# Optimization experiments

Measured on AMD Instinct MI355X. Metric: run time of the kernel, lower is better.

## Reference

```python
import jax, jax.numpy as jnp
import numpy as np

# Static config matching init_kwargs / input_specs
B, C, H, W, T = 2, 128, 32, 32, 32
OUT = 256
WS, SHIFT, HEADS = 4, 2, 8
MLP = 4 * C
N = WS ** 3          # tokens per 4x4x4 window = 64
D_BLOCKS = 4         # depth=2 -> 2 (no-shift, shift) pairs


def _rel_idx():
    coords = np.stack(np.meshgrid(np.arange(WS), np.arange(WS), np.arange(WS), indexing='ij')).reshape(3, -1)
    rel = (coords[:, :, None] - coords[:, None, :]).transpose(1, 2, 0) + (WS - 1)
    return (rel[..., 0] * (2 * WS - 1) ** 2 + rel[..., 1] * (2 * WS - 1) + rel[..., 2]).astype(np.int32)

REL_IDX = jnp.asarray(_rel_idx())  # [N, N]


def _attn_mask():
    # Faithful port of Block.createmask (H,W,T already multiples of WS)
    img = np.zeros((H, W, T))
    sl = (slice(0, -WS), slice(-WS, -SHIFT), slice(-SHIFT, None))
    cnt = 0
    for hs in sl:
        for ws_ in sl:
            for ts in sl:
                img[hs, ws_, ts] = cnt
                cnt += 1
    m = img.reshape(H // WS, WS, W // WS, WS, T // WS, WS).transpose(0, 2, 4, 1, 3, 5).reshape(-1, N)
    am = m[:, None, :] - m[:, :, None]
    return jnp.asarray(np.where(am != 0, -100.0, 0.0).astype(np.float32))  # [nW, N, N]

MASK = _attn_mask()


def _partition(x):  # [b,H,W,T,c] -> [b*nW, N, c]
    b, c = x.shape[0], x.shape[-1]
    x = x.reshape(b, H // WS, WS, W // WS, WS, T // WS, WS, c).transpose(0, 1, 3, 5, 2, 4, 6, 7)
    return x.reshape(-1, N, c)


def _reverse(wins, b, c):  # [b*nW, N, c] -> [b,H,W,T,c]
    x = wins.reshape(b, H // WS, W // WS, T // WS, WS, WS, WS, c).transpose(0, 1, 4, 2, 5, 3, 6, 7)
    return x.reshape(b, H, W, T, c)


def _ln(x, g, b):
    mu = x.mean(-1, keepdims=True)
    var = ((x - mu) ** 2).mean(-1, keepdims=True)
    return (x - mu) / jnp.sqrt(var + 1e-5) * g + b


def _swin(x, shift, g1, b1, qw, qb, pw, pb, rpb, g2, b2, f1w, f1b, f2w, f2b):
    b, L, c = x.shape
    hd = c // HEADS
    scale = hd ** -0.5
    h = _ln(x, g1, b1).reshape(b, H, W, T, c)
    if shift:
        h = jnp.roll(h, (-SHIFT, -SHIFT, -SHIFT), axis=(1, 2, 3))
    win = _partition(h)  # [b*nW, N, c]
    qkv = (win @ qw.T + qb).reshape(-1, N, 3, HEADS, hd).transpose(2, 0, 3, 1, 4)
    q, k, v = qkv[0] * scale, qkv[1], qkv[2]
    attn = jnp.einsum('bhnd,bhmd->bhnm', q, k) + rpb[REL_IDX].transpose(2, 0, 1)[None]
    if shift:
        nW = MASK.shape[0]
        attn = (attn.reshape(b, nW, HEADS, N, N) + MASK[None, :, None]).reshape(-1, HEADS, N, N)
    attn = jax.nn.softmax(attn, axis=-1)
    o = jnp.einsum('bhnm,bhmd->bhnd', attn, v).transpose(0, 2, 1, 3).reshape(-1, N, c)
    o = o @ pw.T + pb
    h = _reverse(o, b, c)
    if shift:
        h = jnp.roll(h, (SHIFT, SHIFT, SHIFT), axis=(1, 2, 3))
    x = x + h.reshape(b, L, c)
    m = jax.nn.gelu(_ln(x, g2, b2) @ f1w.T + f1b, approximate=False)
    return x + (m @ f2w.T + f2b)


def setup_inputs() -> dict:
    key = jax.random.key(0)
    ks = jax.random.split(key, 10)
    r = lambda i, sh, s=0.02: jax.random.normal(ks[i], sh, jnp.float32) * s
    Dn = D_BLOCKS
    return {
        'x': jax.random.normal(ks[0], (B, C, H, W, T), jnp.float32),
        'norm1_g': jnp.ones((Dn, C), jnp.float32), 'norm1_b': jnp.zeros((Dn, C), jnp.float32),
        'qkv_w': r(1, (Dn, 3 * C, C)), 'qkv_b': jnp.zeros((Dn, 3 * C), jnp.float32),
        'proj_w': r(2, (Dn, C, C)), 'proj_b': jnp.zeros((Dn, C), jnp.float32),
        'rpb': r(3, (Dn, (2 * WS - 1) ** 3, HEADS)),
        'norm2_g': jnp.ones((Dn, C), jnp.float32), 'norm2_b': jnp.zeros((Dn, C), jnp.float32),
        'fc1_w': r(4, (Dn, MLP, C)), 'fc1_b': jnp.zeros((Dn, MLP), jnp.float32),
        'fc2_w': r(5, (Dn, C, MLP)), 'fc2_b': jnp.zeros((Dn, C), jnp.float32),
        'dw_w': r(6, (C, 1, 3, 3, 3), 0.1), 'dw_b': jnp.zeros((C,), jnp.float32),
        'pw_w': r(7, (OUT, C, 1, 1, 1), 0.05), 'pw_b': jnp.zeros((OUT,), jnp.float32),
        'bn_g': jnp.ones((OUT,), jnp.float32), 'bn_b': jnp.zeros((OUT,), jnp.float32),
    }


def reference(x, norm1_g, norm1_b, qkv_w, qkv_b, proj_w, proj_b, rpb, norm2_g, norm2_b,
              fc1_w, fc1_b, fc2_w, fc2_b, dw_w, dw_b, pw_w, pw_b, bn_g, bn_b):
    b = x.shape[0]
    t = x.transpose(0, 2, 3, 4, 1).reshape(b, H * W * T, C)  # b (h w t) c
    shifts = [0, SHIFT, 0, SHIFT]
    for i, s in enumerate(shifts):
        t = _swin(t, s, norm1_g[i], norm1_b[i], qkv_w[i], qkv_b[i], proj_w[i], proj_b[i],
                  rpb[i], norm2_g[i], norm2_b[i], fc1_w[i], fc1_b[i], fc2_w[i], fc2_b[i])
    y = t.reshape(b, H, W, T, C).transpose(0, 4, 1, 2, 3)
    # connectBlock: depthwise 3x3x3 conv + pointwise 1x1x1 conv + BatchNorm3d + ReLU
    dn = ('NCDHW', 'OIDHW', 'NCDHW')
    y = jax.lax.conv_general_dilated(y, dw_w, (1, 1, 1), 'SAME', dimension_numbers=dn,
                                     feature_group_count=C) + dw_b[None, :, None, None, None]
    y = jax.lax.conv_general_dilated(y, pw_w, (1, 1, 1), 'SAME', dimension_numbers=dn) + pw_b[None, :, None, None, None]
    mu = y.mean((0, 2, 3, 4), keepdims=True)
    var = ((y - mu) ** 2).mean((0, 2, 3, 4), keepdims=True)
    y = (y - mu) / jnp.sqrt(var + 1e-5) * bn_g[None, :, None, None, None] + bn_b[None, :, None, None, None]
    return jax.nn.relu(y)
```

## Files before the change

kernel.cpp:

```cpp
#include <hip/hip_runtime.h>
#include <hip/hip_bf16.h>
#include <cstddef>
#include <cstdint>

typedef __attribute__((ext_vector_type(8))) short short8;
typedef __attribute__((ext_vector_type(4))) short short4v;
typedef __attribute__((ext_vector_type(4))) float floatx4;
typedef __hip_bfloat16 bf16;

#define HEADS 8
#define TOK   65536
#define OUTC  256

__device__ inline float b2f(short s) {
    union { unsigned u; float f; } x;
    x.u = ((unsigned)(unsigned short)s) << 16;
    return x.f;
}

__device__ inline floatx4 mfma16(short4v a, short4v b, floatx4 c) {
#if __has_builtin(__builtin_amdgcn_mfma_f32_16x16x16bf16_1k)
    return __builtin_amdgcn_mfma_f32_16x16x16bf16_1k(a, b, c, 0, 0, 0);
#else
    floatx4 d;
    asm volatile("v_mfma_f32_16x16x16_bf16 %0, %1, %2, %3\n\ts_nop 7"
                 : "=v"(d) : "v"(a), "v"(b), "v"(c));
    return d;
#endif
}

__global__ __launch_bounds__(256) void transpose_in_kernel(
    const float* __restrict__ x, float* __restrict__ out, float* __restrict__ tstats)
{
    __shared__ float tile[128 * 65];
    int chunk = blockIdx.x;
    int tid = threadIdx.x;
    int b = chunk >> 9;
    int sp0 = (chunk & 511) * 64;
    #pragma unroll
    for (int l = 0; l < 32; ++l) {
        int idx = l * 256 + tid;
        int c = idx >> 6;
        int s = idx & 63;
        tile[c * 65 + s] = x[(((size_t)(b * 128 + c)) << 15) + sp0 + s];
    }
    __syncthreads();
    #pragma unroll
    for (int l = 0; l < 32; ++l) {
        int idx = l * 256 + tid;
        int s = idx >> 7;
        int c = idx & 127;
        out[((size_t)((b << 15) + sp0 + s)) * 128 + c] = tile[c * 65 + s];
    }
    int s = tid >> 2, q = tid & 3;
    float sm = 0.f, sq = 0.f;
    #pragma unroll
    for (int cc = 0; cc < 32; ++cc) {
        float v = tile[(q * 32 + cc) * 65 + s];
        sm += v; sq += v * v;
    }
    sm += __shfl_xor(sm, 1); sq += __shfl_xor(sq, 1);
    sm += __shfl_xor(sm, 2); sq += __shfl_xor(sq, 2);
    if (q == 0) {
        float mu = sm * (1.0f / 128.0f);
        float var = sq * (1.0f / 128.0f) - mu * mu;
        size_t tok = (size_t)(b << 15) + sp0 + s;
        tstats[tok * 2]     = mu;
        tstats[tok * 2 + 1] = rsqrtf(var + 1e-5f);
    }
}

__global__ __launch_bounds__(256) void prep_kernel(
    const float* __restrict__ qkv_w, const float* __restrict__ proj_w,
    const float* __restrict__ fc1_w, const float* __restrict__ fc2_w,
    const float* __restrict__ pw_w, const float* __restrict__ dw_w,
    const float* __restrict__ norm1_g,
    bf16* __restrict__ wbf, float* __restrict__ dwt, float* __restrict__ stats)
{
    int i = blockIdx.x * 256 + threadIdx.x;
    float v;
    if (i < 196608) {
        int layer = i / 49152, k = i & 127;
        v = qkv_w[i] * norm1_g[layer * 128 + k];
    }
    else if (i < 262144)  v = proj_w[i - 196608];
    else if (i < 524288)  v = fc1_w[i - 262144];
    else if (i < 786432)  v = fc2_w[i - 524288];
    else                  v = pw_w[i - 786432];
    wbf[i] = __float2bfloat16(v);
    if (i < 3456) {
        int c = i / 27, k = i % 27;
        dwt[k * 128 + c] = dw_w[i];
    }
    if (i < 512) stats[i] = 0.f;
}

__global__ __launch_bounds__(256) void foldbias_kernel(
    const float* __restrict__ qkv_w, const float* __restrict__ qkv_b,
    const float* __restrict__ norm1_b, float* __restrict__ qkvb)
{
    int t = blockIdx.x * 256 + threadIdx.x;
    if (t >= 1536) return;
    int l = t / 384, n = t % 384;
    const float* wr = qkv_w + (size_t)l * 49152 + n * 128;
    const float* br = norm1_b + l * 128;
    float s = qkv_b[t];
    #pragma unroll 4
    for (int k = 0; k < 128; ++k) s += wr[k] * br[k];
    qkvb[t] = s;
}

__global__ __launch_bounds__(256) void pack_kernel(
    const float* __restrict__ fc1_w, const float* __restrict__ fc2_w,
    bf16* __restrict__ pw1, bf16* __restrict__ pw2)
{
    int t = blockIdx.x * 256 + threadIdx.x;
    int i = t >> 17;
    int rem = t & 131071;
    int type = rem >> 16;
    int idx = rem & 65535;
    int j = idx & 7, lane = (idx >> 3) & 63;
    int ln15 = lane & 15, quad = lane >> 4;
    if (type == 0) {
        int nt = (idx >> 9) & 1, kk = (idx >> 10) & 3, wv = (idx >> 12) & 3, cc = (idx >> 14) & 3;
        int row = cc * 128 + wv * 32 + nt * 16 + ln15;
        int col = kk * 32 + quad * 8 + j;
        pw1[i * 65536 + idx] = __float2bfloat16(fc1_w[(size_t)i * 65536 + row * 128 + col]);
    } else {
        int nt = (idx >> 9) & 1, ks = (idx >> 10) & 3, cc = (idx >> 12) & 3, wv = (idx >> 14) & 3;
        int row = wv * 32 + nt * 16 + ln15;
        int col = cc * 128 + ks * 32 + quad * 8 + j;
        pw2[i * 65536 + idx] = __float2bfloat16(fc2_w[(size_t)i * 65536 + row * 512 + col]);
    }
}

__global__ __launch_bounds__(256) void rpe_expand_kernel(
    const float* __restrict__ rpb, float* __restrict__ rpe, int layer)
{
    int t = blockIdx.x * 256 + threadIdx.x;
    int j = t & 63, i = (t >> 6) & 63, head = (t >> 12) & 7, wt = t >> 15;
    int ih = i >> 4, iw = (i >> 2) & 3, it = i & 3;
    int jh = j >> 4, jw = (j >> 2) & 3, jt = j & 3;
    int ridx = ((ih - jh + 3) * 7 + (iw - jw + 3)) * 7 + (it - jt + 3);
    float v = rpb[layer * 2744 + ridx * 8 + head];
    if (wt) {
        bool ok = true;
        if (wt & 4) ok = ok && ((ih >= 2) == (jh >= 2));
        if (wt & 2) ok = ok && ((iw >= 2) == (jw >= 2));
        if (wt & 1) ok = ok && ((it >= 2) == (jt >= 2));
        if (!ok) v -= 100.f;
    }
    rpe[t] = v;
}

__global__ __launch_bounds__(256) void gemm_bf16_kernel(
    const bf16* __restrict__ A, const bf16* __restrict__ Bw,
    const float* __restrict__ bias, bf16* __restrict__ Cb, float* __restrict__ Cf,
    float* __restrict__ aux, const float* __restrict__ p1, const float* __restrict__ p2,
    int M, int N, int K, int mode, int shift)
{
    __shared__ __align__(16) char smem[34816];
    __shared__ float cs[128];
    __shared__ float cq[128];
    short* As = (short*)smem;
    short* Bs = (short*)(smem + 8192);
    int tid = threadIdx.x;
    int lane = tid & 63, wv = tid >> 6;
    int wm = wv >> 1, wn = wv & 1;
    int ln15 = lane & 15, quad = lane >> 4;
    int q8 = quad * 8;
    int nBase = blockIdx.x * 128;
    int mBase = blockIdx.y * 128;
    floatx4 acc[4][4] = {};

    if (mode == 4 && tid < 128) { cs[tid] = 0.f; cq[tid] = 0.f; }

    int srow = tid >> 2, scb = tid & 3;

    int toks[2]; float tmu[2], trs[2];
    if (mode == 0) {
        #pragma unroll
        for (int i = 0; i < 2; ++i) {
            int m = mBase + srow + i * 64;
            int n = m & 63, w = (m >> 6) & 511, b = m >> 15;
            int ih = n >> 4, iw = (n >> 2) & 3, it = n & 3;
            int wh = w >> 6, ww = (w >> 3) & 7, wt = w & 7;
            int h  = (wh * 4 + ih + shift) & 31;
            int w2 = (ww * 4 + iw + shift) & 31;
            int t  = (wt * 4 + it + shift) & 31;
            toks[i] = (b << 15) + ((h * 32 + w2) * 32 + t);
            tmu[i] = aux[(size_t)toks[i] * 2];
            trs[i] = aux[(size_t)toks[i] * 2 + 1];
        }
    }

    for (int k0 = 0; k0 < K; k0 += 32) {
        if (mode == 0) {
            int cb = k0 + scb * 8;
            #pragma unroll
            for (int i = 0; i < 2; ++i) {
                const float* xr = Cf + (size_t)toks[i] * 128 + cb;
                float4 a0 = *(const float4*)xr;
                float4 a1 = *(const float4*)(xr + 4);
                float mu = tmu[i], rs = trs[i];
                __align__(16) bf16 pk[8];
                pk[0] = __float2bfloat16((a0.x - mu) * rs);
                pk[1] = __float2bfloat16((a0.y - mu) * rs);
                pk[2] = __float2bfloat16((a0.z - mu) * rs);
                pk[3] = __float2bfloat16((a0.w - mu) * rs);
                pk[4] = __float2bfloat16((a1.x - mu) * rs);
                pk[5] = __float2bfloat16((a1.y - mu) * rs);
                pk[6] = __float2bfloat16((a1.z - mu) * rs);
                pk[7] = __float2bfloat16((a1.w - mu) * rs);
                ((uint4*)As)[i * 256 + tid] = *(const uint4*)pk;
                ((uint4*)Bs)[i * 256 + tid] =
                    *(const uint4*)(Bw + (size_t)(nBase + srow + i * 64) * K + cb);
            }
        } else {
            #pragma unroll
            for (int i = 0; i < 2; ++i) {
                int row = srow + i * 64;
                ((uint4*)As)[i * 256 + tid] =
                    *(const uint4*)(A + (size_t)(mBase + row) * K + k0 + scb * 8);
                ((uint4*)Bs)[i * 256 + tid] =
                    *(const uint4*)(Bw + (size_t)(nBase + row) * K + k0 + scb * 8);
            }
        }
        __syncthreads();
        short8 af[4], bfr[4];
        #pragma unroll
        for (int mt = 0; mt < 4; ++mt)
            af[mt] = *(const short8*)&As[(wm * 64 + mt * 16 + ln15) * 32 + q8];
        #pragma unroll
        for (int nt = 0; nt < 4; ++nt)
            bfr[nt] = *(const short8*)&Bs[(wn * 64 + nt * 16 + ln15) * 32 + q8];
        #pragma unroll
        for (int mt = 0; mt < 4; ++mt)
            #pragma unroll
            for (int nt = 0; nt < 4; ++nt)
                acc[mt][nt] = __builtin_amdgcn_mfma_f32_16x16x32_bf16(
                    af[mt], bfr[nt], acc[mt][nt], 0, 0, 0);
        __syncthreads();
    }

    if (mode == 4) {
        #pragma unroll
        for (int nt = 0; nt < 4; ++nt) {
            int nl = wn * 64 + nt * 16 + ln15;
            float bs = bias[nBase + nl];
            float s = 0.f, sq = 0.f;
            #pragma unroll
            for (int mt = 0; mt < 4; ++mt)
                #pragma unroll
                for (int r = 0; r < 4; ++r) {
                    float v = acc[mt][nt][r] + bs;
                    s += v; sq += v * v;
                }
            atomicAdd(&cs[nl], s);
            atomicAdd(&cq[nl], sq);
        }
        __syncthreads();
        if (tid < 128) {
            atomicAdd(&aux[nBase + tid], cs[tid]);
            atomicAdd(&aux[256 + nBase + tid], cq[tid]);
        }
        return;
    }

    if (mode == 0) {
        bf16* estage = (bf16*)smem;
        float qsc = (nBase == 0) ? 0.25f : 1.0f;
        #pragma unroll
        for (int mt = 0; mt < 4; ++mt)
            #pragma unroll
            for (int nt = 0; nt < 4; ++nt)
                #pragma unroll
                for (int r = 0; r < 4; ++r) {
                    int row = wm * 64 + mt * 16 + quad * 4 + r;
                    int col = wn * 64 + nt * 16 + ln15;
                    estage[row * 136 + col] =
                        __float2bfloat16((acc[mt][nt][r] + bias[nBase + col]) * qsc);
                }
        __syncthreads();
        int row = tid >> 1, hf = tid & 1;
        #pragma unroll
        for (int j = 0; j < 4; ++j) {
            int col = hf * 64 + j * 16;
            *(uint4*)(Cb + (size_t)(mBase + row) * N + nBase + col) =
                *(const uint4*)&estage[row * 136 + col];
            *(uint4*)(Cb + (size_t)(mBase + row) * N + nBase + col + 8) =
                *(const uint4*)&estage[row * 136 + col + 8];
        }
        return;
    }

    if (mode == 2) {
        float* fstage = (float*)smem;
        #pragma unroll
        for (int hf = 0; hf < 2; ++hf) {
            if (wm == hf) {
                #pragma unroll
                for (int mt = 0; mt < 4; ++mt)
                    #pragma unroll
                    for (int nt = 0; nt < 4; ++nt)
                        #pragma unroll
                        for (int r = 0; r < 4; ++r) {
                            int ml = mt * 16 + quad * 4 + r;
                            int col = wn * 64 + nt * 16 + ln15;
                            fstage[ml * 132 + col] = acc[mt][nt][r] + bias[col];
                        }
            }
            __syncthreads();
            int tl = tid >> 2, part = tid & 3;
            int g = mBase + hf * 64 + tl;
            int n_ = g & 63, w = (g >> 6) & 511, b = g >> 15;
            int ih = n_ >> 4, iw = (n_ >> 2) & 3, it = n_ & 3;
            int wh = w >> 6, ww = (w >> 3) & 7, wt = w & 7;
            int h  = (wh * 4 + ih + shift) & 31;
            int w2 = (ww * 4 + iw + shift) & 31;
            int t  = (wt * 4 + it + shift) & 31;
            size_t tok = ((size_t)b << 15) + ((h * 32 + w2) * 32 + t);
            float* dst = aux + tok * 128 + part * 32;
            #pragma unroll
            for (int j = 0; j < 8; ++j) {
                float4 a = *(float4*)(dst + j * 4);
                float4 l = *(const float4*)&fstage[tl * 132 + part * 32 + j * 4];
                a.x += l.x; a.y += l.y; a.z += l.z; a.w += l.w;
                *(float4*)(dst + j * 4) = a;
            }
            __syncthreads();
        }
        return;
    }

    {
        float* fstage = (float*)smem;
        int b = mBase >> 15, sp0 = mBase & 32767;
        #pragma unroll
        for (int hf = 0; hf < 2; ++hf) {
            if (wn == hf) {
                #pragma unroll
                for (int nt = 0; nt < 4; ++nt) {
                    int ncol = nt * 16 + ln15;
                    int nn = nBase + hf * 64 + ncol;
                    float mean = aux[nn] * (1.0f / 65536.0f);
                    float var  = aux[256 + nn] * (1.0f / 65536.0f) - mean * mean;
                    float sc = rsqrtf(var + 1e-5f) * p1[nn];
                    float off = p2[nn] + bias[nn] * sc - mean * sc;
                    #pragma unroll
                    for (int mt = 0; mt < 4; ++mt)
                        #pragma unroll
                        for (int r = 0; r < 4; ++r) {
                            int ml = wm * 64 + mt * 16 + quad * 4 + r;
                            float y = acc[mt][nt][r] * sc + off;
                            fstage[ncol * 132 + ml] = fmaxf(y, 0.f);
                        }
                }
            }
            __syncthreads();
            int nl = tid >> 2, part = tid & 3;
            int nn = nBase + hf * 64 + nl;
            float* dst = Cf + (((size_t)(b * 256 + nn)) << 15) + sp0 + part * 32;
            #pragma unroll
            for (int j = 0; j < 8; ++j)
                *(float4*)(dst + j * 4) = *(const float4*)&fstage[nl * 132 + part * 32 + j * 4];
            __syncthreads();
        }
    }
}

__global__ __launch_bounds__(256, 4) void mlp_kernel(
    float* __restrict__ xbuf, const float* __restrict__ g, const float* __restrict__ bta,
    const bf16* __restrict__ pw1, const float* __restrict__ b1,
    const bf16* __restrict__ pw2, const float* __restrict__ b2,
    bf16* __restrict__ xout16, float* __restrict__ tstats)
{
    __shared__ __align__(16) bf16 smem[64 * 136 * 2];
    bf16* aln  = smem;
    bf16* hidc = smem + 64 * 136;
    float* ostage = (float*)smem;
    int tid = threadIdx.x;
    int lane = tid & 63, wv = tid >> 6;
    int ln15 = lane & 15, quad = lane >> 4;
    int q8 = quad * 8;
    size_t tok0 = (size_t)blockIdx.x * 64;

    #pragma unroll
    for (int itk = 0; itk < 16; ++itk) {
        int t = wv * 16 + itk;
        const float* xp = xbuf + (tok0 + t) * 128;
        float v0 = xp[lane], v1 = xp[lane + 64];
        float s = v0 + v1, sq = v0 * v0 + v1 * v1;
        #pragma unroll
        for (int o = 32; o > 0; o >>= 1) { s += __shfl_xor(s, o); sq += __shfl_xor(sq, o); }
        float mu  = s * (1.0f / 128.0f);
        float var = sq * (1.0f / 128.0f) - mu * mu;
        float rs  = rsqrtf(var + 1e-5f);
        aln[t * 136 + lane]      = __float2bfloat16((v0 - mu) * rs * g[lane]      + bta[lane]);
        aln[t * 136 + lane + 64] = __float2bfloat16((v1 - mu) * rs * g[lane + 64] + bta[lane + 64]);
    }
    __syncthreads();

    floatx4 acc2[4][2] = {};
    #pragma unroll
    for (int cc = 0; cc < 4; ++cc) {
        floatx4 acc[4][2] = {};
        const bf16* p1w = pw1 + (size_t)(cc * 4 + wv) * 4096;
        #pragma unroll
        for (int kk = 0; kk < 4; ++kk) {
            short8 af[4], bfr[2];
            #pragma unroll
            for (int mt = 0; mt < 4; ++mt)
                af[mt] = *(const short8*)&aln[(mt * 16 + ln15) * 136 + kk * 32 + q8];
            #pragma unroll
            for (int nt = 0; nt < 2; ++nt)
                bfr[nt] = *(const short8*)(p1w + kk * 1024 + nt * 512 + lane * 8);
            #pragma unroll
            for (int mt = 0; mt < 4; ++mt)
                #pragma unroll
                for (int nt = 0; nt < 2; ++nt)
                    acc[mt][nt] = __builtin_amdgcn_mfma_f32_16x16x32_bf16(
                        af[mt], bfr[nt], acc[mt][nt], 0, 0, 0);
        }
        if (cc) __syncthreads();
        #pragma unroll
        for (int mt = 0; mt < 4; ++mt)
            #pragma unroll
            for (int nt = 0; nt < 2; ++nt)
                #pragma unroll
                for (int r = 0; r < 4; ++r) {
                    int m = mt * 16 + quad * 4 + r;
                    int ncl = wv * 32 + nt * 16 + ln15;
                    float v = acc[mt][nt][r] + b1[cc * 128 + ncl];
                    float u = v * (0.7978845608f + 0.0356774081f * v * v);
                    v = v * __builtin_amdgcn_rcpf(1.f + __expf(-2.f * u));
                    hidc[m * 136 + ncl] = __float2bfloat16(v);
                }
        __syncthreads();
        const bf16* p2w = pw2 + (size_t)(wv * 4 + cc) * 4096;
        #pragma unroll
        for (int ks = 0; ks < 4; ++ks) {
            short8 af[4], bfr[2];
            #pragma unroll
            for (int mt = 0; mt < 4; ++mt)
                af[mt] = *(const short8*)&hidc[(mt * 16 + ln15) * 136 + ks * 32 + q8];
            #pragma unroll
            for (int nt = 0; nt < 2; ++nt)
                bfr[nt] = *(const short8*)(p2w + ks * 1024 + nt * 512 + lane * 8);
            #pragma unroll
            for (int mt = 0; mt < 4; ++mt)
                #pragma unroll
                for (int nt = 0; nt < 2; ++nt)
                    acc2[mt][nt] = __builtin_amdgcn_mfma_f32_16x16x32_bf16(
                        af[mt], bfr[nt], acc2[mt][nt], 0, 0, 0);
        }
    }
    __syncthreads();

    #pragma unroll
    for (int mt = 0; mt < 4; ++mt)
        #pragma unroll
        for (int nt = 0; nt < 2; ++nt)
            #pragma unroll
            for (int r = 0; r < 4; ++r) {
                int m = mt * 16 + quad * 4 + r;
                int n = wv * 32 + nt * 16 + ln15;
                ostage[m * 132 + n] = acc2[mt][nt][r] + b2[n];
            }
    __syncthreads();

    #pragma unroll
    for (int jj = 0; jj < 8; ++jj) {
        int idx = (jj * 256 + tid) * 4;
        int t = idx >> 7, c = idx & 127;
        float4 v = *(const float4*)(xbuf + tok0 * 128 + idx);
        float4 o = *(const float4*)&ostage[t * 132 + c];
        v.x += o.x; v.y += o.y; v.z += o.z; v.w += o.w;
        *(float4*)(xbuf + tok0 * 128 + idx) = v;
        if (xout16) {
            __align__(8) bf16 hh[4];
            hh[0] = __float2bfloat16(v.x); hh[1] = __float2bfloat16(v.y);
            hh[2] = __float2bfloat16(v.z); hh[3] = __float2bfloat16(v.w);
            *(uint2*)(xout16 + tok0 * 128 + idx) = *(const uint2*)hh;
        }
        float ps = v.x + v.y + v.z + v.w;
        float pq = v.x * v.x + v.y * v.y + v.z * v.z + v.w * v.w;
        #pragma unroll
        for (int o2 = 16; o2 > 0; o2 >>= 1) {
            ps += __shfl_xor(ps, o2); pq += __shfl_xor(pq, o2);
        }
        if ((tid & 31) == 0) {
            float mu = ps * (1.0f / 128.0f);
            float var = pq * (1.0f / 128.0f) - mu * mu;
            size_t tok = tok0 + t;
            tstats[tok * 2]     = mu;
            tstats[tok * 2 + 1] = rsqrtf(var + 1e-5f);
        }
    }
}

__global__ __launch_bounds__(256, 3) void attn_mfma_kernel(
    const bf16* __restrict__ qkv, const float* __restrict__ rpe,
    bf16* __restrict__ outp, int shift)
{
    __shared__ __align__(16) short qs[64 * 392];
    int tid = threadIdx.x;
    int lane = tid & 63, wv = tid >> 6;
    int ln15 = lane & 15, quad = lane >> 4;
    int win = blockIdx.x;
    size_t tok0 = (size_t)win * 64;

    const short* gq = (const short*)qkv + tok0 * 384;
    #pragma unroll
    for (int l = 0; l < 12; ++l) {
        int idx = l * 256 + tid;
        int r = idx / 48, c = idx - r * 48;
        *(uint4*)&qs[r * 392 + c * 8] = *(const uint4*)&gq[r * 384 + c * 8];
    }
    int w = win & 511;
    int wtype = 0;
    if (shift)
        wtype = (((w >> 6) == 7) << 2) | ((((w >> 3) & 7) == 7) << 1) | (int)((w & 7) == 7);
    const float* rpw = rpe + ((size_t)(wtype * 8) << 12);
    __syncthreads();

    floatx4 oacc[2][4];
    #pragma unroll
    for (int hh = 0; hh < 2; ++hh) {
        int head = wv * 2 + hh;
        const float* rph = rpw + ((size_t)head << 12);

        floatx4 acc[4][4];
        #pragma unroll
        for (int jt = 0; jt < 4; ++jt)
            #pragma unroll
            for (int it = 0; it < 4; ++it)
                acc[jt][it] = *(const floatx4*)&rph[(it * 16 + ln15) * 64 + jt * 16 + quad * 4];

        short4v qf[4], kf[4];
        #pragma unroll
        for (int it = 0; it < 4; ++it)
            qf[it] = *(const short4v*)&qs[(it * 16 + ln15) * 392 + head * 16 + quad * 4];
        #pragma unroll
        for (int jt = 0; jt < 4; ++jt)
            kf[jt] = *(const short4v*)&qs[(jt * 16 + ln15) * 392 + 128 + head * 16 + quad * 4];

        #pragma unroll
        for (int jt = 0; jt < 4; ++jt)
            #pragma unroll
            for (int it = 0; it < 4; ++it)
                acc[jt][it] = mfma16(kf[jt], qf[it], acc[jt][it]);

        short4v pf[4][4];
        #pragma unroll
        for (int it = 0; it < 4; ++it) {
            float m = -1e30f;
            #pragma unroll
            for (int jt = 0; jt < 4; ++jt)
                #pragma unroll
                for (int r = 0; r < 4; ++r) m = fmaxf(m, acc[jt][it][r]);
            m = fmaxf(m, __shfl_xor(m, 16));
            m = fmaxf(m, __shfl_xor(m, 32));
            float s = 0.f;
            #pragma unroll
            for (int jt = 0; jt < 4; ++jt)
                #pragma unroll
                for (int r = 0; r < 4; ++r) {
                    float e = __expf(acc[jt][it][r] - m);
                    acc[jt][it][r] = e; s += e;
                }
            s += __shfl_xor(s, 16);
            s += __shfl_xor(s, 32);
            float inv = 1.0f / s;
            #pragma unroll
            for (int jt = 0; jt < 4; ++jt) {
                __align__(8) bf16 pb[4];
                #pragma unroll
                for (int r = 0; r < 4; ++r)
                    pb[r] = __float2bfloat16(acc[jt][it][r] * inv);
                pf[jt][it] = *(const short4v*)pb;
            }
        }

        short4v vf[4];
        #pragma unroll
        for (int jt = 0; jt < 4; ++jt)
            #pragma unroll
            for (int jj = 0; jj < 4; ++jj)
                vf[jt][jj] = qs[(jt * 16 + quad * 4 + jj) * 392 + 256 + head * 16 + ln15];

        #pragma unroll
        for (int it = 0; it < 4; ++it) {
            floatx4 o = {0.f, 0.f, 0.f, 0.f};
            #pragma unroll
            for (int jt = 0; jt < 4; ++jt)
                o = mfma16(vf[jt], pf[jt][it], o);
            oacc[hh][it] = o;
        }
    }
    __syncthreads();

    short* ob = qs;
    #pragma unroll
    for (int hh = 0; hh < 2; ++hh)
        #pragma unroll
        for (int it = 0; it < 4; ++it) {
            __align__(8) bf16 t4[4];
            #pragma unroll
            for (int r = 0; r < 4; ++r) t4[r] = __float2bfloat16(oacc[hh][it][r]);
            *(short4v*)&ob[(it * 16 + ln15) * 136 + (wv * 2 + hh) * 16 + quad * 4] =
                *(const short4v*)t4;
        }
    __syncthreads();

    short* po = (short*)outp + tok0 * 128;
    #pragma unroll
    for (int l = 0; l < 4; ++l) {
        int idx = l * 256 + tid;
        int r = idx >> 4, c = idx & 15;
        *(uint4*)&po[r * 128 + c * 8] = *(const uint4*)&ob[r * 136 + c * 8];
    }
}

__global__ __launch_bounds__(256) void dwconv_kernel(
    const bf16* __restrict__ x, const float* __restrict__ dwt,
    const float* __restrict__ bias, bf16* __restrict__ out)
{
    int blk = blockIdx.x;
    int b = blk >> 9;
    int h = (blk >> 4) & 31;
    int w = ((blk & 15) << 1) | (threadIdx.x >> 7);
    int tid = threadIdx.x & 127;
    int c0 = (tid & 31) * 4;
    int t0 = (tid >> 5) * 8;

    float4 acc[8];
    float4 bs = *(const float4*)&bias[c0];
    #pragma unroll
    for (int o = 0; o < 8; ++o) acc[o] = bs;

    #pragma unroll
    for (int kh = 0; kh < 3; ++kh) {
        int hh = h + kh - 1;
        if (hh < 0 || hh > 31) continue;
        #pragma unroll
        for (int kw = 0; kw < 3; ++kw) {
            int ww = w + kw - 1;
            if (ww < 0 || ww > 31) continue;
            const short* px = (const short*)x +
                ((size_t)(b << 15) + (hh * 32 + ww) * 32) * 128 + c0;
            float4 v[10];
            #pragma unroll
            for (int u = 0; u < 10; ++u) {
                int tt = t0 - 1 + u;
                if (tt >= 0 && tt < 32) {
                    short4v s4 = *(const short4v*)(px + (size_t)tt * 128);
                    v[u].x = b2f(s4[0]); v[u].y = b2f(s4[1]);
                    v[u].z = b2f(s4[2]); v[u].w = b2f(s4[3]);
                } else {
                    v[u].x = v[u].y = v[u].z = v[u].w = 0.f;
                }
            }
            int kb = kh * 9 + kw * 3;
            float4 w0 = *(const float4*)&dwt[(kb + 0) * 128 + c0];
            float4 w1 = *(const float4*)&dwt[(kb + 1) * 128 + c0];
            float4 w2 = *(const float4*)&dwt[(kb + 2) * 128 + c0];
            #pragma unroll
            for (int o = 0; o < 8; ++o) {
                acc[o].x += v[o].x * w0.x + v[o + 1].x * w1.x + v[o + 2].x * w2.x;
                acc[o].y += v[o].y * w0.y + v[o + 1].y * w1.y + v[o + 2].y * w2.y;
                acc[o].z += v[o].z * w0.z + v[o + 1].z * w1.z + v[o + 2].z * w2.z;
                acc[o].w += v[o].w * w0.w + v[o + 1].w * w1.w + v[o + 2].w * w2.w;
            }
        }
    }
    short* po = (short*)out + ((size_t)(b << 15) + (h * 32 + w) * 32 + t0) * 128 + c0;
    #pragma unroll
    for (int o = 0; o < 8; ++o) {
        __align__(8) bf16 h4[4];
        h4[0] = __float2bfloat16(acc[o].x);
        h4[1] = __float2bfloat16(acc[o].y);
        h4[2] = __float2bfloat16(acc[o].z);
        h4[3] = __float2bfloat16(acc[o].w);
        *(uint2*)(po + (size_t)o * 128) = *(const uint2*)h4;
    }
}

extern "C" void kernel_launch(void* const* d_in, const int* in_sizes, int n_in,
                              void* d_out, int out_size, void* d_ws, size_t ws_size,
                              hipStream_t stream)
{
    const float* x_in    = (const float*)d_in[0];
    const float* norm1_g = (const float*)d_in[1];
    const float* norm1_b = (const float*)d_in[2];
    const float* qkv_w   = (const float*)d_in[3];
    const float* qkv_b   = (const float*)d_in[4];
    const float* proj_w  = (const float*)d_in[5];
    const float* proj_b  = (const float*)d_in[6];
    const float* rpb     = (const float*)d_in[7];
    const float* norm2_g = (const float*)d_in[8];
    const float* norm2_b = (const float*)d_in[9];
    const float* fc1_w   = (const float*)d_in[10];
    const float* fc1_b   = (const float*)d_in[11];
    const float* fc2_w   = (const float*)d_in[12];
    const float* fc2_b   = (const float*)d_in[13];
    const float* dw_w    = (const float*)d_in[14];
    const float* dw_b    = (const float*)d_in[15];
    const float* pw_w    = (const float*)d_in[16];
    const float* pw_b    = (const float*)d_in[17];
    const float* bn_g    = (const float*)d_in[18];
    const float* bn_b    = (const float*)d_in[19];
    float* out = (float*)d_out;

    char* ws = (char*)d_ws;
    float* xbuf   = (float*)ws;
    bf16*  wbf    = (bf16*)(ws + 33554432ULL);
    float* dwt    = (float*)(ws + 35651584ULL);
    float* stats  = (float*)(ws + 35717120ULL);
    float* qkvb   = (float*)(ws + 35719168ULL);
    bf16*  pw1    = (bf16*)(ws + 35782656ULL);
    bf16*  pw2    = (bf16*)(ws + 36306944ULL);
    float* tstats = (float*)(ws + 36831232ULL);
    bf16*  lnbuf  = (bf16*)(ws + 37748736ULL);
    bf16*  attnbuf= (bf16*)(ws + 54525952ULL);
    bf16*  qkvbuf = (bf16*)(ws + 71303168ULL);
    bf16*  dwbuf  = attnbuf;
    bf16*  dcbuf  = lnbuf;
    float* rpe    = (float*)lnbuf;

    bf16* wqkv  = wbf;
    bf16* wproj = wbf + 196608;
    bf16* wpw   = wbf + 786432;

    hipLaunchKernelGGL(prep_kernel, dim3(3200), dim3(256), 0, stream,
                       qkv_w, proj_w, fc1_w, fc2_w, pw_w, dw_w, norm1_g,
                       wbf, dwt, stats);
    hipLaunchKernelGGL(foldbias_kernel, dim3(6), dim3(256), 0, stream,
                       qkv_w, qkv_b, norm1_b, qkvb);
    hipLaunchKernelGGL(pack_kernel, dim3(2048), dim3(256), 0, stream,
                       fc1_w, fc2_w, pw1, pw2);
    hipLaunchKernelGGL(transpose_in_kernel, dim3(1024), dim3(256), 0, stream,
                       x_in, xbuf, tstats);

    const int shifts[4] = {0, 2, 0, 2};
    for (int i = 0; i < 4; ++i) {
        int s = shifts[i];
        hipLaunchKernelGGL(gemm_bf16_kernel, dim3(3, TOK / 128), dim3(256), 0, stream,
                           (const bf16*)nullptr, wqkv + (size_t)i * 49152, qkvb + i * 384,
                           qkvbuf, xbuf, tstats,
                           (const float*)nullptr, (const float*)nullptr,
                           TOK, 384, 128, 0, s);
        hipLaunchKernelGGL(rpe_expand_kernel, dim3(s ? 1024 : 128), dim3(256), 0, stream,
                           rpb, rpe, i);
        hipLaunchKernelGGL(attn_mfma_kernel, dim3(TOK / 64), dim3(256), 0, stream,
                           qkvbuf, rpe, attnbuf, s);
        hipLaunchKernelGGL(gemm_bf16_kernel, dim3(1, TOK / 128), dim3(256), 0, stream,
                           attnbuf, wproj + (size_t)i * 16384, proj_b + i * 128,
                           (bf16*)nullptr, (float*)nullptr, xbuf,
                           (const float*)nullptr, (const float*)nullptr,
                           TOK, 128, 128, 2, s);
        hipLaunchKernelGGL(mlp_kernel, dim3(TOK / 64), dim3(256), 0, stream,
                           xbuf, norm2_g + i * 128, norm2_b + i * 128,
                           pw1 + (size_t)i * 65536, fc1_b + i * 512,
                           pw2 + (size_t)i * 65536, fc2_b + i * 128,
                           (i == 3) ? dwbuf : (bf16*)nullptr, tstats);
    }

    hipLaunchKernelGGL(dwconv_kernel, dim3(1024), dim3(256), 0, stream,
                       dwbuf, dwt, dw_b, dcbuf);
    hipLaunchKernelGGL(gemm_bf16_kernel, dim3(OUTC / 128, TOK / 128), dim3(256), 0, stream,
                       dcbuf, wpw, pw_b,
                       (bf16*)nullptr, (float*)nullptr, stats,
                       (const float*)nullptr, (const float*)nullptr,
                       TOK, OUTC, 128, 4, 0);
    hipLaunchKernelGGL(gemm_bf16_kernel, dim3(OUTC / 128, TOK / 128), dim3(256), 0, stream,
                       dcbuf, wpw, pw_b,
                       (bf16*)nullptr, out, stats,
                       bn_g, bn_b,
                       TOK, OUTC, 128, 5, 0);
}
```

Baseline: 751.0 us.

## Fuse attention output projection and residual into MLP kernel; fold LN2 affine into fc1

Removes the separate proj GEMM launch (mode 2), which did a read-modify-write of the fp32 residual stream. The MLP kernel now gathers the window-ordered attention output for its token tile, applies the pre-packed proj weights with MFMA, adds the residual, and reuses the result for LN2 and for the final residual add. The LN2 gamma and beta are folded into the fc1 weights and a precomputed bias, so the kernel only normalizes. This saves one full fp32 pass over the activations and one launch. In exchange the MLP kernel does more work and uses more registers (xm held across phases), which may lower occupancy.

Measured after the change: 699.0 us. -6.9%, faster.

```diff
diff --git a/kernel.cpp b/kernel.cpp
--- a/kernel.cpp
+++ b/kernel.cpp
@@ -83,7 +83,15 @@
         int layer = i / 49152, k = i & 127;
         v = qkv_w[i] * norm1_g[layer * 128 + k];
     }
-    else if (i < 262144)  v = proj_w[i - 196608];
+    else if (i < 262144) {
+        int jd = i - 196608;
+        int layer = jd >> 14, idx = jd & 16383;
+        int j = idx & 7, lane = (idx >> 3) & 63;
+        int nt = (idx >> 9) & 1, ks = (idx >> 10) & 3, wvv = (idx >> 12) & 3;
+        int row = wvv * 32 + nt * 16 + (lane & 15);
+        int col = ks * 32 + (lane >> 4) * 8 + j;
+        v = proj_w[layer * 16384 + row * 128 + col];
+    }
     else if (i < 524288)  v = fc1_w[i - 262144];
     else if (i < 786432)  v = fc2_w[i - 524288];
     else                  v = pw_w[i - 786432];
@@ -97,21 +105,34 @@
 
 __global__ __launch_bounds__(256) void foldbias_kernel(
     const float* __restrict__ qkv_w, const float* __restrict__ qkv_b,
-    const float* __restrict__ norm1_b, float* __restrict__ qkvb)
+    const float* __restrict__ norm1_b,
+    const float* __restrict__ fc1_w, const float* __restrict__ fc1_b,
+    const float* __restrict__ norm2_b, float* __restrict__ fb)
 {
     int t = blockIdx.x * 256 + threadIdx.x;
-    if (t >= 1536) return;
-    int l = t / 384, n = t % 384;
-    const float* wr = qkv_w + (size_t)l * 49152 + n * 128;
-    const float* br = norm1_b + l * 128;
-    float s = qkv_b[t];
-    #pragma unroll 4
-    for (int k = 0; k < 128; ++k) s += wr[k] * br[k];
-    qkvb[t] = s;
+    if (t < 1536) {
+        int l = t / 384, n = t % 384;
+        const float* wr = qkv_w + (size_t)l * 49152 + n * 128;
+        const float* br = norm1_b + l * 128;
+        float s = qkv_b[t];
+        #pragma unroll 4
+        for (int k = 0; k < 128; ++k) s += wr[k] * br[k];
+        fb[t] = s;
+    } else if (t < 3584) {
+        int u = t - 1536;
+        int l = u >> 9, n = u & 511;
+        const float* wr = fc1_w + (size_t)l * 65536 + n * 128;
+        const float* br = norm2_b + l * 128;
+        float s = fc1_b[l * 512 + n];
+        #pragma unroll 4
+        for (int k = 0; k < 128; ++k) s += wr[k] * br[k];
+        fb[t] = s;
+    }
 }
 
 __global__ __launch_bounds__(256) void pack_kernel(
     const float* __restrict__ fc1_w, const float* __restrict__ fc2_w,
+    const float* __restrict__ norm2_g,
     bf16* __restrict__ pw1, bf16* __restrict__ pw2)
 {
     int t = blockIdx.x * 256 + threadIdx.x;
@@ -125,7 +146,8 @@
         int nt = (idx >> 9) & 1, kk = (idx >> 10) & 3, wv = (idx >> 12) & 3, cc = (idx >> 14) & 3;
         int row = cc * 128 + wv * 32 + nt * 16 + ln15;
         int col = kk * 32 + quad * 8 + j;
-        pw1[i * 65536 + idx] = __float2bfloat16(fc1_w[(size_t)i * 65536 + row * 128 + col]);
+        pw1[i * 65536 + idx] = __float2bfloat16(
+            fc1_w[(size_t)i * 65536 + row * 128 + col] * norm2_g[i * 128 + col]);
     } else {
         int nt = (idx >> 9) & 1, ks = (idx >> 10) & 3, cc = (idx >> 12) & 3, wv = (idx >> 14) & 3;
         int row = wv * 32 + nt * 16 + ln15;
@@ -290,45 +312,6 @@
                 *(const uint4*)&estage[row * 136 + col];
             *(uint4*)(Cb + (size_t)(mBase + row) * N + nBase + col + 8) =
                 *(const uint4*)&estage[row * 136 + col + 8];
-        }
-        return;
-    }
-
-    if (mode == 2) {
-        float* fstage = (float*)smem;
-        #pragma unroll
-        for (int hf = 0; hf < 2; ++hf) {
-            if (wm == hf) {
-                #pragma unroll
-                for (int mt = 0; mt < 4; ++mt)
-                    #pragma unroll
-                    for (int nt = 0; nt < 4; ++nt)
-                        #pragma unroll
-                        for (int r = 0; r < 4; ++r) {
-                            int ml = mt * 16 + quad * 4 + r;
-                            int col = wn * 64 + nt * 16 + ln15;
-                            fstage[ml * 132 + col] = acc[mt][nt][r] + bias[col];
-                        }
-            }
-            __syncthreads();
-            int tl = tid >> 2, part = tid & 3;
-            int g = mBase + hf * 64 + tl;
-            int n_ = g & 63, w = (g >> 6) & 511, b = g >> 15;
-            int ih = n_ >> 4, iw = (n_ >> 2) & 3, it = n_ & 3;
-            int wh = w >> 6, ww = (w >> 3) & 7, wt = w & 7;
-            int h  = (wh * 4 + ih + shift) & 31;
-            int w2 = (ww * 4 + iw + shift) & 31;
-            int t  = (wt * 4 + it + shift) & 31;
-            size_t tok = ((size_t)b << 15) + ((h * 32 + w2) * 32 + t);
-            float* dst = aux + tok * 128 + part * 32;
-            #pragma unroll
-            for (int j = 0; j < 8; ++j) {
-                float4 a = *(float4*)(dst + j * 4);
-                float4 l = *(const float4*)&fstage[tl * 132 + part * 32 + j * 4];
-                a.x += l.x; a.y += l.y; a.z += l.z; a.w += l.w;
-                *(float4*)(dst + j * 4) = a;
-            }
-            __syncthreads();
         }
         return;
     }
@@ -370,10 +353,11 @@
 }
 
 __global__ __launch_bounds__(256, 4) void mlp_kernel(
-    float* __restrict__ xbuf, const float* __restrict__ g, const float* __restrict__ bta,
+    float* __restrict__ xbuf, const bf16* __restrict__ attnbuf,
+    const bf16* __restrict__ ppw, const float* __restrict__ pb,
     const bf16* __restrict__ pw1, const float* __restrict__ b1,
     const bf16* __restrict__ pw2, const float* __restrict__ b2,
-    bf16* __restrict__ xout16, float* __restrict__ tstats)
+    bf16* __restrict__ xout16, float* __restrict__ tstats, int shift)
 {
     __shared__ __align__(16) bf16 smem[64 * 136 * 2];
     bf16* aln  = smem;
@@ -383,21 +367,86 @@
     int lane = tid & 63, wv = tid >> 6;
     int ln15 = lane & 15, quad = lane >> 4;
     int q8 = quad * 8;
-    size_t tok0 = (size_t)blockIdx.x * 64;
-
-    #pragma unroll
-    for (int itk = 0; itk < 16; ++itk) {
-        int t = wv * 16 + itk;
-        const float* xp = xbuf + (tok0 + t) * 128;
-        float v0 = xp[lane], v1 = xp[lane + 64];
-        float s = v0 + v1, sq = v0 * v0 + v1 * v1;
-        #pragma unroll
-        for (int o = 32; o > 0; o >>= 1) { s += __shfl_xor(s, o); sq += __shfl_xor(sq, o); }
-        float mu  = s * (1.0f / 128.0f);
-        float var = sq * (1.0f / 128.0f) - mu * mu;
-        float rs  = rsqrtf(var + 1e-5f);
-        aln[t * 136 + lane]      = __float2bfloat16((v0 - mu) * rs * g[lane]      + bta[lane]);
-        aln[t * 136 + lane + 64] = __float2bfloat16((v1 - mu) * rs * g[lane + 64] + bta[lane + 64]);
+    int blk = blockIdx.x;
+    size_t tok0 = (size_t)blk * 64;
+    int b = blk >> 9, h = (blk >> 4) & 31, wpair = blk & 15;
+
+    #pragma unroll
+    for (int l = 0; l < 4; ++l) {
+        int q = l * 256 + tid;
+        int row = q >> 4, c16 = q & 15;
+        int w2 = wpair * 2 + (row >> 5), t = row & 31;
+        int hs = (h - shift) & 31, ws = (w2 - shift) & 31, ts = (t - shift) & 31;
+        int wr = (b << 15) + (((hs >> 2) * 64 + ((ws >> 2) << 3) + (ts >> 2)) << 6)
+               + ((hs & 3) * 16 + ((ws & 3) << 2) + (ts & 3));
+        *(uint4*)&aln[row * 136 + c16 * 8] =
+            *(const uint4*)((const short*)attnbuf + (size_t)wr * 128 + c16 * 8);
+    }
+    __syncthreads();
+
+    floatx4 accp[4][2] = {};
+    #pragma unroll
+    for (int ks = 0; ks < 4; ++ks) {
+        short8 af[4], bfr[2];
+        #pragma unroll
+        for (int mt = 0; mt < 4; ++mt)
+            af[mt] = *(const short8*)&aln[(mt * 16 + ln15) * 136 + ks * 32 + q8];
+        #pragma unroll
+        for (int nt = 0; nt < 2; ++nt)
+            bfr[nt] = *(const short8*)(ppw + wv * 4096 + ks * 1024 + nt * 512 + lane * 8);
+        #pragma unroll
+        for (int mt = 0; mt < 4; ++mt)
+            #pragma unroll
+            for (int nt = 0; nt < 2; ++nt)
+                accp[mt][nt] = __builtin_amdgcn_mfma_f32_16x16x32_bf16(
+                    af[mt], bfr[nt], accp[mt][nt], 0, 0, 0);
+    }
+    __syncthreads();
+
+    #pragma unroll
+    for (int mt = 0; mt < 4; ++mt)
+        #pragma unroll
+        for (int nt = 0; nt < 2; ++nt)
+            #pragma unroll
+            for (int r = 0; r < 4; ++r) {
+                int m = mt * 16 + quad * 4 + r;
+                int n = wv * 32 + nt * 16 + ln15;
+                ostage[m * 132 + n] = accp[mt][nt][r] + pb[n];
+            }
+    __syncthreads();
+
+    float4 xm[8];
+    #pragma unroll
+    for (int jj = 0; jj < 8; ++jj) {
+        int idx = (jj * 256 + tid) * 4;
+        int t = idx >> 7, c = idx & 127;
+        float4 v = *(const float4*)(xbuf + tok0 * 128 + idx);
+        float4 o = *(const float4*)&ostage[t * 132 + c];
+        v.x += o.x; v.y += o.y; v.z += o.z; v.w += o.w;
+        xm[jj] = v;
+    }
+    __syncthreads();
+
+    #pragma unroll
+    for (int jj = 0; jj < 8; ++jj) {
+        int idx = (jj * 256 + tid) * 4;
+        int t = idx >> 7, c = idx & 127;
+        float4 v = xm[jj];
+        float ps = v.x + v.y + v.z + v.w;
+        float pq = v.x * v.x + v.y * v.y + v.z * v.z + v.w * v.w;
+        #pragma unroll
+        for (int o2 = 16; o2 > 0; o2 >>= 1) {
+            ps += __shfl_xor(ps, o2); pq += __shfl_xor(pq, o2);
+        }
+        float mu = ps * (1.0f / 128.0f);
+        float var = pq * (1.0f / 128.0f) - mu * mu;
+        float rs = rsqrtf(var + 1e-5f);
+        __align__(8) bf16 hh[4];
+        hh[0] = __float2bfloat16((v.x - mu) * rs);
+        hh[1] = __float2bfloat16((v.y - mu) * rs);
+        hh[2] = __float2bfloat16((v.z - mu) * rs);
+        hh[3] = __float2bfloat16((v.w - mu) * rs);
+        *(uint2*)&aln[t * 136 + c] = *(const uint2*)hh;
     }
     __syncthreads();
 
@@ -473,7 +522,7 @@
     for (int jj = 0; jj < 8; ++jj) {
         int idx = (jj * 256 + tid) * 4;
         int t = idx >> 7, c = idx & 127;
-        float4 v = *(const float4*)(xbuf + tok0 * 128 + idx);
+        float4 v = xm[jj];
         float4 o = *(const float4*)&ostage[t * 132 + c];
         v.x += o.x; v.y += o.y; v.z += o.z; v.w += o.w;
         *(float4*)(xbuf + tok0 * 128 + idx) = v;
@@ -717,28 +766,28 @@
     bf16*  wbf    = (bf16*)(ws + 33554432ULL);
     float* dwt    = (float*)(ws + 35651584ULL);
     float* stats  = (float*)(ws + 35717120ULL);
-    float* qkvb   = (float*)(ws + 35719168ULL);
+    float* fb     = (float*)(ws + 35719168ULL);
     bf16*  pw1    = (bf16*)(ws + 35782656ULL);
     bf16*  pw2    = (bf16*)(ws + 36306944ULL);
     float* tstats = (float*)(ws + 36831232ULL);
     bf16*  lnbuf  = (bf16*)(ws + 37748736ULL);
     bf16*  attnbuf= (bf16*)(ws + 54525952ULL);
     bf16*  qkvbuf = (bf16*)(ws + 71303168ULL);
-    bf16*  dwbuf  = attnbuf;
+    bf16*  dwbuf  = qkvbuf;
     bf16*  dcbuf  = lnbuf;
     float* rpe    = (float*)lnbuf;
 
     bf16* wqkv  = wbf;
-    bf16* wproj = wbf + 196608;
+    bf16* pproj = wbf + 196608;
     bf16* wpw   = wbf + 786432;
 
     hipLaunchKernelGGL(prep_kernel, dim3(3200), dim3(256), 0, stream,
                        qkv_w, proj_w, fc1_w, fc2_w, pw_w, dw_w, norm1_g,
                        wbf, dwt, stats);
-    hipLaunchKernelGGL(foldbias_kernel, dim3(6), dim3(256), 0, stream,
-                       qkv_w, qkv_b, norm1_b, qkvb);
+    hipLaunchKernelGGL(foldbias_kernel, dim3(14), dim3(256), 0, stream,
+                       qkv_w, qkv_b, norm1_b, fc1_w, fc1_b, norm2_b, fb);
     hipLaunchKernelGGL(pack_kernel, dim3(2048), dim3(256), 0, stream,
-                       fc1_w, fc2_w, pw1, pw2);
+                       fc1_w, fc2_w, norm2_g, pw1, pw2);
     hipLaunchKernelGGL(transpose_in_kernel, dim3(1024), dim3(256), 0, stream,
                        x_in, xbuf, tstats);
 
@@ -746,7 +795,7 @@
     for (int i = 0; i < 4; ++i) {
         int s = shifts[i];
         hipLaunchKernelGGL(gemm_bf16_kernel, dim3(3, TOK / 128), dim3(256), 0, stream,
-                           (const bf16*)nullptr, wqkv + (size_t)i * 49152, qkvb + i * 384,
+                           (const bf16*)nullptr, wqkv + (size_t)i * 49152, fb + i * 384,
                            qkvbuf, xbuf, tstats,
                            (const float*)nullptr, (const float*)nullptr,
                            TOK, 384, 128, 0, s);
@@ -754,16 +803,12 @@
                            rpb, rpe, i);
         hipLaunchKernelGGL(attn_mfma_kernel, dim3(TOK / 64), dim3(256), 0, stream,
                            qkvbuf, rpe, attnbuf, s);
-        hipLaunchKernelGGL(gemm_bf16_kernel, dim3(1, TOK / 128), dim3(256), 0, stream,
-                           attnbuf, wproj + (size_t)i * 16384, proj_b + i * 128,
-                           (bf16*)nullptr, (float*)nullptr, xbuf,
-                           (const float*)nullptr, (const float*)nullptr,
-                           TOK, 128, 128, 2, s);
         hipLaunchKernelGGL(mlp_kernel, dim3(TOK / 64), dim3(256), 0, stream,
-                           xbuf, norm2_g + i * 128, norm2_b + i * 128,
-                           pw1 + (size_t)i * 65536, fc1_b + i * 512,
+                           xbuf, attnbuf,
+                           pproj + (size_t)i * 16384, proj_b + i * 128,
+                           pw1 + (size_t)i * 65536, fb + 1536 + i * 512,
                            pw2 + (size_t)i * 65536, fc2_b + i * 128,
-                           (i == 3) ? dwbuf : (bf16*)nullptr, tstats);
+                           (i == 3) ? dwbuf : (bf16*)nullptr, tstats, s);
     }
 
     hipLaunchKernelGGL(dwconv_kernel, dim3(1024), dim3(256), 0, stream,
```
